# Kernel tuning notes

Measured on AMD Instinct MI355X. Metric: run time of the kernel, lower is better.

The kernel has to match this reference:

```python
import jax, jax.numpy as jnp
import numpy as np

B, INP, OUP, FGROUP, H, W = 32, 256, 256, 8, 64, 64
CG = INP // FGROUP  # channels per group in GLGF fc1 layers


def conv3x3(x, w):
    # x: (N,1,H,W), w: (1,1,3,3); stride 1, padding 1 (SAME)
    return jax.lax.conv_general_dilated(
        x, w, window_strides=(1, 1), padding='SAME',
        dimension_numbers=('NCHW', 'OIHW', 'NCHW'))


def setup_inputs() -> dict:
    key = jax.random.key(0)
    ks = jax.random.split(key, 8)
    return {
        'x': jax.random.normal(ks[0], (B, INP, H, W), dtype=jnp.float32),
        # GLGF params (all 1x1 convs, bias=False), stored as dense matrices
        'w1l': jax.random.normal(ks[1], (FGROUP, CG, CG), dtype=jnp.float32) * 0.05,   # wn_fc1_l (groups=fgroup)
        'w1g1': jax.random.normal(ks[2], (FGROUP, CG), dtype=jnp.float32) * 0.05,      # wn_fc1_g1 (inp->fgroup, groups=fgroup)
        'w1g2': jax.random.normal(ks[3], (INP, FGROUP), dtype=jnp.float32) * 0.05,     # wn_fc1_g2 (fgroup->inp dense)
        'w2l': jax.random.normal(ks[4], (INP, OUP), dtype=jnp.float32) * 0.05,         # wn_fc2_l (groups=inp): input ch i -> oup outputs
        'w2g': jax.random.normal(ks[5], (INP,), dtype=jnp.float32) * 0.05,             # wn_fc2_g (inp->1 dense)
        'conv1_w': jax.random.normal(ks[6], (1, 1, 3, 3), dtype=jnp.float32) * 0.1,
        'conv2_w': jax.random.normal(ks[7], (1, 1, 3, 3), dtype=jnp.float32) * 0.1,
    }


def reference(x, w1l, w1g1, w1g2, w2l, w2g, conv1_w, conv2_w):
    b, c, h, w_ = x.shape
    fgroup, cg, _ = w1l.shape
    oup = w2l.shape[1]

    # adaptive_avg_pool2d(x, (1,1)) -> (B, inp) descriptor
    g = x.mean(axis=(2, 3))                                   # (B, inp)
    gg = g.reshape(b, fgroup, cg)

    # GLGF: fc1_l (grouped) + fc1_g2(fc1_g1) (squeeze to fgroup then expand)
    local = jnp.einsum('bgi,goi->bgo', gg, w1l).reshape(b, c)  # (B, inp)
    glob = jnp.einsum('bgi,gi->bg', gg, w1g1) @ w1g2.T         # (B, inp)
    s = jax.nn.sigmoid(local + glob)                           # (B, inp)

    # fc2_l (groups=inp): torch channel order is (input_ch g, out j) -> g*oup + j
    # fc2_g adds a per-sample scalar to every channel
    xw = s[:, :, None] * w2l + (s @ w2g)[:, None, None]        # (B, inp, oup)
    # WA_1Conv reinterprets the flat (oup*inp) channels as (oup, inp)
    Wdyn = xw.reshape(b, oup, c)                               # (B, oup, inp)

    # grouped conv with groups=batch, ksize=1 == per-sample matmul
    y = jnp.einsum('bihw,boi->bohw', x, Wdyn)                  # (B, oup, H, W)

    # channel gating: mean over channels -> conv3x3 -> sigmoid -> conv3x3
    cmap = y.mean(axis=1, keepdims=True)                       # (B, 1, H, W)
    cmap = conv3x3(cmap, conv1_w)
    cmap = jax.nn.sigmoid(cmap)
    cmap = conv3x3(cmap, conv2_w)
    return y * cmap
```

## Files before the change

kernel.cpp:

```cpp
#include <hip/hip_runtime.h>
#include <hip/hip_bf16.h>

typedef float  f32x4  __attribute__((ext_vector_type(4)));
typedef short  bf16x8 __attribute__((ext_vector_type(8)));

__device__ __forceinline__ short f2bf(float f) {
    union { __hip_bfloat16 h; short s; } u;
    u.h = __float2bfloat16(f);
    return u.s;
}

__device__ __forceinline__ void gload_lds16(const void* g, void* l) {
    __builtin_amdgcn_global_load_lds(
        (const __attribute__((address_space(1))) unsigned int*)g,
        (__attribute__((address_space(3))) unsigned int*)l, 16, 0, 0);
}

__global__ __launch_bounds__(256) void transpose_kernel(const float* __restrict__ x,
                                                        short* __restrict__ xt,
                                                        float* __restrict__ gpart) {
    const int pchunk = blockIdx.x;
    const int c0 = blockIdx.y * 64;
    const int b  = blockIdx.z;
    const int tid = threadIdx.x;
    const int row = tid >> 2;
    const int quad = tid & 3;
    const int p0 = pchunk * 64;

    __shared__ short tile[64 * 72];

    const float* xr = x + ((size_t)(b * 256 + c0 + row)) * 4096 + p0 + quad * 16;
    float sum = 0.f;
    #pragma unroll
    for (int it = 0; it < 4; ++it) {
        float4 v = *reinterpret_cast<const float4*>(xr + it * 4);
        sum += v.x + v.y + v.z + v.w;
        int pb = quad * 16 + it * 4;
        tile[(pb + 0) * 72 + row] = f2bf(v.x);
        tile[(pb + 1) * 72 + row] = f2bf(v.y);
        tile[(pb + 2) * 72 + row] = f2bf(v.z);
        tile[(pb + 3) * 72 + row] = f2bf(v.w);
    }
    sum += __shfl_xor(sum, 1, 64);
    sum += __shfl_xor(sum, 2, 64);
    if (quad == 0) gpart[(size_t)(b * 256 + c0 + row) * 64 + pchunk] = sum;
    __syncthreads();
    int p = tid >> 2;
    const int4* src = reinterpret_cast<const int4*>(&tile[p * 72 + quad * 16]);
    int4* dst = reinterpret_cast<int4*>(xt + ((size_t)b * 4096 + p0 + p) * 256 + c0 + quad * 16);
    dst[0] = src[0];
    dst[1] = src[1];
}

__global__ __launch_bounds__(256) void prep_kernel(
    const float* __restrict__ gpart, const float* __restrict__ w1l,
    const float* __restrict__ w1g1, const float* __restrict__ w1g2,
    const float* __restrict__ w2l, const float* __restrict__ w2g,
    float* __restrict__ s_out, float* __restrict__ t_out,
    float* __restrict__ q_out, short* __restrict__ w2l_bf) {
    int b = blockIdx.x;
    int tid = threadIdx.x;
    if (b >= 32) {
        int seg = b - 32;
        const float* src = w2l + seg * 4096;
        short* dst = w2l_bf + seg * 4096;
        #pragma unroll
        for (int it = 0; it < 4; ++it) {
            float4 v = *reinterpret_cast<const float4*>(src + it * 1024 + tid * 4);
            short4 o;
            o.x = f2bf(v.x); o.y = f2bf(v.y); o.z = f2bf(v.z); o.w = f2bf(v.w);
            *reinterpret_cast<short4*>(dst + it * 1024 + tid * 4) = o;
        }
        return;
    }
    __shared__ float gs[256];
    __shared__ float zs[8];
    __shared__ float ss[256];
    __shared__ float red[4];
    {
        const float4* gp = reinterpret_cast<const float4*>(gpart + (size_t)(b * 256 + tid) * 64);
        float acc = 0.f;
        #pragma unroll
        for (int j = 0; j < 16; ++j) { float4 v = gp[j]; acc += v.x + v.y + v.z + v.w; }
        gs[tid] = acc * (1.0f / 4096.0f);
    }
    __syncthreads();
    if (tid < 8) {
        float z = 0.f;
        for (int i = 0; i < 32; ++i) z += gs[tid * 32 + i] * w1g1[tid * 32 + i];
        zs[tid] = z;
    }
    __syncthreads();
    int grp = tid >> 5, o = tid & 31;
    float local = 0.f;
    #pragma unroll 4
    for (int i = 0; i < 32; ++i) local += gs[grp * 32 + i] * w1l[grp * 1024 + o * 32 + i];
    float glob = 0.f;
    #pragma unroll
    for (int gg = 0; gg < 8; ++gg) glob += zs[gg] * w1g2[tid * 8 + gg];
    float sv = 1.0f / (1.0f + expf(-(local + glob)));
    ss[tid] = sv;
    s_out[b * 256 + tid] = sv;
    float tv = sv * w2g[tid];
    #pragma unroll
    for (int off = 32; off; off >>= 1) tv += __shfl_down(tv, off, 64);
    if ((tid & 63) == 0) red[tid >> 6] = tv;
    __syncthreads();
    float tb = red[0] + red[1] + red[2] + red[3];
    if (tid == 0) t_out[b] = tb;
    float v = 0.f;
    for (int o2 = 0; o2 < 256; ++o2) v += ss[o2] * w2l[o2 * 256 + tid];
    q_out[b * 256 + tid] = v * (1.0f / 256.0f) + tb;
}

__global__ __launch_bounds__(256) void cmap0_kernel(const float* __restrict__ x,
                                                    const float* __restrict__ q,
                                                    float* __restrict__ cmap0,
                                                    float* __restrict__ xsum) {
    int b = blockIdx.y;
    int p = blockIdx.x * 512 + threadIdx.x * 2;
    __shared__ float qs[256];
    qs[threadIdx.x] = q[b * 256 + threadIdx.x];
    __syncthreads();
    const float* xb = x + (size_t)b * 256 * 4096;
    float a0 = 0.f, a1 = 0.f, s0 = 0.f, s1 = 0.f;
    #pragma unroll 4
    for (int i = 0; i < 256; ++i) {
        float2 v = *reinterpret_cast<const float2*>(xb + (size_t)i * 4096 + p);
        float qi = qs[i];
        a0 += qi * v.x; a1 += qi * v.y;
        s0 += v.x;      s1 += v.y;
    }
    cmap0[b * 4096 + p] = a0; cmap0[b * 4096 + p + 1] = a1;
    xsum[b * 4096 + p] = s0;  xsum[b * 4096 + p + 1] = s1;
}

__global__ __launch_bounds__(256) void convs_kernel(const float* __restrict__ in,
                                                    const float* __restrict__ w9a,
                                                    const float* __restrict__ w9b,
                                                    float* __restrict__ out) {
    int b = blockIdx.x;
    int tid = threadIdx.x;
    __shared__ float img[4096];
    __shared__ float mid[4096];
    float wa[9], wb[9];
    #pragma unroll
    for (int i = 0; i < 9; ++i) { wa[i] = w9a[i]; wb[i] = w9b[i]; }
    {
        const float4* ip = reinterpret_cast<const float4*>(in + (size_t)b * 4096);
        float4* lp = reinterpret_cast<float4*>(img);
        #pragma unroll
        for (int it = 0; it < 4; ++it) lp[it * 256 + tid] = ip[it * 256 + tid];
    }
    __syncthreads();
    #pragma unroll
    for (int it = 0; it < 16; ++it) {
        int pix = it * 256 + tid;
        int y = pix >> 6, x0 = pix & 63;
        float acc = 0.f;
        #pragma unroll
        for (int dy = -1; dy <= 1; ++dy)
            #pragma unroll
            for (int dx = -1; dx <= 1; ++dx) {
                int yy = y + dy, xx = x0 + dx;
                if (yy >= 0 && yy < 64 && xx >= 0 && xx < 64)
                    acc += img[yy * 64 + xx] * wa[(dy + 1) * 3 + (dx + 1)];
            }
        mid[pix] = 1.0f / (1.0f + expf(-acc));
    }
    __syncthreads();
    #pragma unroll
    for (int it = 0; it < 16; ++it) {
        int pix = it * 256 + tid;
        int y = pix >> 6, x0 = pix & 63;
        float acc = 0.f;
        #pragma unroll
        for (int dy = -1; dy <= 1; ++dy)
            #pragma unroll
            for (int dx = -1; dx <= 1; ++dx) {
                int yy = y + dy, xx = x0 + dx;
                if (yy >= 0 && yy < 64 && xx >= 0 && xx < 64)
                    acc += mid[yy * 64 + xx] * wb[(dy + 1) * 3 + (dx + 1)];
            }
        out[(size_t)b * 4096 + pix] = acc;
    }
}

__global__ __launch_bounds__(512) void gemm_epi_kernel(
    const short* __restrict__ xt, const short* __restrict__ w2l_bf,
    const float* __restrict__ s, const float* __restrict__ t,
    const float* __restrict__ xsum, const float* __restrict__ cmap,
    float* __restrict__ out) {
    const int b  = blockIdx.z;
    const int p0 = blockIdx.x * 64;
    const int tid  = threadIdx.x;
    const int lane = tid & 63;
    const int w    = tid >> 6;
    const int wm = w >> 1, wn = w & 1;

    __shared__ short Alds[256 * 64];
    __shared__ short Xlds[64 * 64];

    const int sl   = (lane & 7) ^ (lane >> 3);
    const int lrow = lane >> 3;

    f32x4 acc[4][2] = {};

    for (int ks = 0; ks < 256; ks += 64) {
        #pragma unroll
        for (int j = 0; j < 4; ++j) {
            int chunk = w * 4 + j;
            int row = chunk * 8 + lrow;
            gload_lds16(w2l_bf + (size_t)row * 256 + ks + sl * 8,
                        (char*)Alds + chunk * 1024);
        }
        {
            int prow = w * 8 + lrow;
            gload_lds16(xt + ((size_t)b * 4096 + p0 + prow) * 256 + ks + sl * 8,
                        (char*)Xlds + w * 1024);
        }
        __syncthreads();
        #pragma unroll
        for (int kk = 0; kk < 2; ++kk) {
            bf16x8 af[4], bfr[2];
            const int ss = kk * 4 + (lane >> 4);
            #pragma unroll
            for (int m = 0; m < 4; ++m) {
                int o = wm * 64 + m * 16 + (lane & 15);
                af[m] = *reinterpret_cast<const bf16x8*>(
                    (char*)Alds + o * 128 + ((ss ^ (lane & 7)) * 16));
            }
            #pragma unroll
            for (int n = 0; n < 2; ++n) {
                int p = wn * 32 + n * 16 + (lane & 15);
                bfr[n] = *reinterpret_cast<const bf16x8*>(
                    (char*)Xlds + p * 128 + ((ss ^ (lane & 7)) * 16));
            }
            #pragma unroll
            for (int m = 0; m < 4; ++m)
                #pragma unroll
                for (int n = 0; n < 2; ++n)
                    acc[m][n] = __builtin_amdgcn_mfma_f32_16x16x32_bf16(af[m], bfr[n], acc[m][n], 0, 0, 0);
        }
        __syncthreads();
    }
    const float tb = t[b];
    #pragma unroll
    for (int n = 0; n < 2; ++n) {
        int p = p0 + wn * 32 + n * 16 + (lane & 15);
        float xs = xsum[b * 4096 + p];
        float cm = cmap[b * 4096 + p];
        float txs = tb * xs;
        #pragma unroll
        for (int m = 0; m < 4; ++m) {
            #pragma unroll
            for (int r = 0; r < 4; ++r) {
                int o = wm * 64 + m * 16 + (lane >> 4) * 4 + r;
                float yv = s[b * 256 + o] * acc[m][n][r] + txs;
                out[((size_t)b * 256 + o) * 4096 + p] = yv * cm;
            }
        }
    }
}

extern "C" void kernel_launch(void* const* d_in, const int* in_sizes, int n_in,
                              void* d_out, int out_size, void* d_ws, size_t ws_size,
                              hipStream_t stream) {
    const float* x       = (const float*)d_in[0];
    const float* w1l     = (const float*)d_in[1];
    const float* w1g1    = (const float*)d_in[2];
    const float* w1g2    = (const float*)d_in[3];
    const float* w2l     = (const float*)d_in[4];
    const float* w2g     = (const float*)d_in[5];
    const float* conv1_w = (const float*)d_in[6];
    const float* conv2_w = (const float*)d_in[7];
    float* out = (float*)d_out;

    float* wsf   = (float*)d_ws;
    float* s     = wsf;
    float* t     = wsf + 8192;
    float* q     = wsf + 8256;
    float* cmap0 = wsf + 16448;
    float* xsum  = wsf + 147520;
    float* cmap  = wsf + 278592;
    float* gpart = wsf + 409664;
    short* w2l_bf = (short*)(wsf + 933952);
    short* xt     = (short*)(wsf + 966720);

    transpose_kernel<<<dim3(64, 4, 32), 256, 0, stream>>>(x, xt, gpart);
    prep_kernel<<<48, 256, 0, stream>>>(gpart, w1l, w1g1, w1g2, w2l, w2g, s, t, q, w2l_bf);
    cmap0_kernel<<<dim3(8, 32), 256, 0, stream>>>(x, q, cmap0, xsum);
    convs_kernel<<<32, 256, 0, stream>>>(cmap0, conv1_w, conv2_w, cmap);
    gemm_epi_kernel<<<dim3(64, 1, 32), 512, 0, stream>>>(xt, w2l_bf, s, t, xsum, cmap, out);
}
```

Measured before the change: 144.0 us.

## Split cmap0 channel reduction across blocks and vectorize transpose LDS packing

The cmap0 reduction over 256 channels is split into 4 channel partitions per sample, giving 512 blocks instead of 256 and using float4 loads. Partial results are summed later in the convs and GEMM epilogue kernels. The transpose kernel now packs two channels' bf16 values into 32-bit words in a swizzled LDS tile, replacing scattered 16-bit stores. The cost is extra partial-buffer traffic and workspace, and more reads in the consumer kernels.

```diff
diff --git a/kernel.cpp b/kernel.cpp
--- a/kernel.cpp
+++ b/kernel.cpp
@@ -23,33 +23,48 @@
     const int c0 = blockIdx.y * 64;
     const int b  = blockIdx.z;
     const int tid = threadIdx.x;
-    const int row = tid >> 2;
-    const int quad = tid & 3;
+    const int cpair = tid >> 3;
+    const int poct  = tid & 7;
     const int p0 = pchunk * 64;
 
-    __shared__ short tile[64 * 72];
-
-    const float* xr = x + ((size_t)(b * 256 + c0 + row)) * 4096 + p0 + quad * 16;
-    float sum = 0.f;
-    #pragma unroll
-    for (int it = 0; it < 4; ++it) {
-        float4 v = *reinterpret_cast<const float4*>(xr + it * 4);
-        sum += v.x + v.y + v.z + v.w;
-        int pb = quad * 16 + it * 4;
-        tile[(pb + 0) * 72 + row] = f2bf(v.x);
-        tile[(pb + 1) * 72 + row] = f2bf(v.y);
-        tile[(pb + 2) * 72 + row] = f2bf(v.z);
-        tile[(pb + 3) * 72 + row] = f2bf(v.w);
-    }
-    sum += __shfl_xor(sum, 1, 64);
-    sum += __shfl_xor(sum, 2, 64);
-    if (quad == 0) gpart[(size_t)(b * 256 + c0 + row) * 64 + pchunk] = sum;
-    __syncthreads();
-    int p = tid >> 2;
-    const int4* src = reinterpret_cast<const int4*>(&tile[p * 72 + quad * 16]);
-    int4* dst = reinterpret_cast<int4*>(xt + ((size_t)b * 4096 + p0 + p) * 256 + c0 + quad * 16);
-    dst[0] = src[0];
-    dst[1] = src[1];
+    __shared__ unsigned int tile[64 * 32];
+
+    const float* rowA = x + ((size_t)(b * 256 + c0 + 2 * cpair)) * 4096 + p0 + poct * 8;
+    const float* rowB = rowA + 4096;
+    float av[8], bv[8];
+    *reinterpret_cast<float4*>(&av[0]) = *reinterpret_cast<const float4*>(rowA);
+    *reinterpret_cast<float4*>(&av[4]) = *reinterpret_cast<const float4*>(rowA + 4);
+    *reinterpret_cast<float4*>(&bv[0]) = *reinterpret_cast<const float4*>(rowB);
+    *reinterpret_cast<float4*>(&bv[4]) = *reinterpret_cast<const float4*>(rowB + 4);
+
+    float sA = 0.f, sB = 0.f;
+    #pragma unroll
+    for (int e = 0; e < 8; ++e) { sA += av[e]; sB += bv[e]; }
+    sA += __shfl_xor(sA, 1, 64); sA += __shfl_xor(sA, 2, 64); sA += __shfl_xor(sA, 4, 64);
+    sB += __shfl_xor(sB, 1, 64); sB += __shfl_xor(sB, 2, 64); sB += __shfl_xor(sB, 4, 64);
+    if (poct == 0) {
+        gpart[((size_t)(b * 256 + c0 + 2 * cpair)) * 64 + pchunk] = sA;
+        gpart[((size_t)(b * 256 + c0 + 2 * cpair + 1)) * 64 + pchunk] = sB;
+    }
+
+    const int s = cpair >> 2, w = cpair & 3;
+    #pragma unroll
+    for (int e = 0; e < 8; ++e) {
+        int p = poct * 8 + e;
+        unsigned int u = (unsigned int)(unsigned short)f2bf(av[e]) |
+                         ((unsigned int)(unsigned short)f2bf(bv[e]) << 16);
+        tile[p * 32 + ((s ^ poct) << 2) + w] = u;
+    }
+    __syncthreads();
+
+    const int so = tid & 7;
+    #pragma unroll
+    for (int h = 0; h < 2; ++h) {
+        int p = (tid >> 3) + h * 32;
+        int sp = so ^ ((p >> 3) & 7);
+        uint4 v = *reinterpret_cast<const uint4*>(&tile[p * 32 + sp * 4]);
+        *reinterpret_cast<uint4*>(xt + ((size_t)b * 4096 + p0 + p) * 256 + c0 + so * 8) = v;
+    }
 }
 
 __global__ __launch_bounds__(256) void prep_kernel(
@@ -115,27 +130,27 @@
 
 __global__ __launch_bounds__(256) void cmap0_kernel(const float* __restrict__ x,
                                                     const float* __restrict__ q,
-                                                    float* __restrict__ cmap0,
-                                                    float* __restrict__ xsum) {
-    int b = blockIdx.y;
-    int p = blockIdx.x * 512 + threadIdx.x * 2;
-    __shared__ float qs[256];
-    qs[threadIdx.x] = q[b * 256 + threadIdx.x];
-    __syncthreads();
-    const float* xb = x + (size_t)b * 256 * 4096;
-    float a0 = 0.f, a1 = 0.f, s0 = 0.f, s1 = 0.f;
-    #pragma unroll 4
-    for (int i = 0; i < 256; ++i) {
-        float2 v = *reinterpret_cast<const float2*>(xb + (size_t)i * 4096 + p);
-        float qi = qs[i];
-        a0 += qi * v.x; a1 += qi * v.y;
-        s0 += v.x;      s1 += v.y;
-    }
-    cmap0[b * 4096 + p] = a0; cmap0[b * 4096 + p + 1] = a1;
-    xsum[b * 4096 + p] = s0;  xsum[b * 4096 + p + 1] = s1;
-}
-
-__global__ __launch_bounds__(256) void convs_kernel(const float* __restrict__ in,
+                                                    float* __restrict__ cmap0p,
+                                                    float* __restrict__ xsump) {
+    const int part = blockIdx.y;
+    const int b = blockIdx.z;
+    const int p = blockIdx.x * 1024 + threadIdx.x * 4;
+    __shared__ float qs[64];
+    if (threadIdx.x < 64) qs[threadIdx.x] = q[b * 256 + part * 64 + threadIdx.x];
+    __syncthreads();
+    const float* xb = x + ((size_t)(b * 256 + part * 64)) * 4096 + p;
+    f32x4 a = {0.f, 0.f, 0.f, 0.f}, sm = {0.f, 0.f, 0.f, 0.f};
+    #pragma unroll 8
+    for (int i = 0; i < 64; ++i) {
+        f32x4 v = *reinterpret_cast<const f32x4*>(xb + (size_t)i * 4096);
+        a += qs[i] * v;
+        sm += v;
+    }
+    *reinterpret_cast<f32x4*>(cmap0p + ((size_t)(part * 32 + b)) * 4096 + p) = a;
+    *reinterpret_cast<f32x4*>(xsump  + ((size_t)(part * 32 + b)) * 4096 + p) = sm;
+}
+
+__global__ __launch_bounds__(256) void convs_kernel(const float* __restrict__ cmap0p,
                                                     const float* __restrict__ w9a,
                                                     const float* __restrict__ w9b,
                                                     float* __restrict__ out) {
@@ -147,10 +162,15 @@
     #pragma unroll
     for (int i = 0; i < 9; ++i) { wa[i] = w9a[i]; wb[i] = w9b[i]; }
     {
-        const float4* ip = reinterpret_cast<const float4*>(in + (size_t)b * 4096);
-        float4* lp = reinterpret_cast<float4*>(img);
-        #pragma unroll
-        for (int it = 0; it < 4; ++it) lp[it * 256 + tid] = ip[it * 256 + tid];
+        #pragma unroll
+        for (int it = 0; it < 4; ++it) {
+            int idx = it * 256 + tid;
+            f32x4 v = {0.f, 0.f, 0.f, 0.f};
+            #pragma unroll
+            for (int part = 0; part < 4; ++part)
+                v += *reinterpret_cast<const f32x4*>(cmap0p + ((size_t)(part * 32 + b)) * 4096 + idx * 4);
+            *reinterpret_cast<f32x4*>(&img[idx * 4]) = v;
+        }
     }
     __syncthreads();
     #pragma unroll
@@ -189,7 +209,7 @@
 __global__ __launch_bounds__(512) void gemm_epi_kernel(
     const short* __restrict__ xt, const short* __restrict__ w2l_bf,
     const float* __restrict__ s, const float* __restrict__ t,
-    const float* __restrict__ xsum, const float* __restrict__ cmap,
+    const float* __restrict__ xsump, const float* __restrict__ cmap,
     float* __restrict__ out) {
     const int b  = blockIdx.z;
     const int p0 = blockIdx.x * 64;
@@ -248,7 +268,10 @@
     #pragma unroll
     for (int n = 0; n < 2; ++n) {
         int p = p0 + wn * 32 + n * 16 + (lane & 15);
-        float xs = xsum[b * 4096 + p];
+        float xs = 0.f;
+        #pragma unroll
+        for (int part = 0; part < 4; ++part)
+            xs += xsump[((size_t)(part * 32 + b)) * 4096 + p];
         float cm = cmap[b * 4096 + p];
         float txs = tb * xs;
         #pragma unroll
@@ -276,20 +299,20 @@
     const float* conv2_w = (const float*)d_in[7];
     float* out = (float*)d_out;
 
-    float* wsf   = (float*)d_ws;
-    float* s     = wsf;
-    float* t     = wsf + 8192;
-    float* q     = wsf + 8256;
-    float* cmap0 = wsf + 16448;
-    float* xsum  = wsf + 147520;
-    float* cmap  = wsf + 278592;
-    float* gpart = wsf + 409664;
-    short* w2l_bf = (short*)(wsf + 933952);
-    short* xt     = (short*)(wsf + 966720);
+    float* wsf    = (float*)d_ws;
+    float* s      = wsf;
+    float* t      = wsf + 8192;
+    float* q      = wsf + 8256;
+    float* cmap0p = wsf + 16448;
+    float* xsump  = wsf + 540736;
+    float* cmap   = wsf + 1065024;
+    float* gpart  = wsf + 1196096;
+    short* w2l_bf = (short*)(wsf + 1720384);
+    short* xt     = (short*)(wsf + 1753152);
 
     transpose_kernel<<<dim3(64, 4, 32), 256, 0, stream>>>(x, xt, gpart);
     prep_kernel<<<48, 256, 0, stream>>>(gpart, w1l, w1g1, w1g2, w2l, w2g, s, t, q, w2l_bf);
-    cmap0_kernel<<<dim3(8, 32), 256, 0, stream>>>(x, q, cmap0, xsum);
-    convs_kernel<<<32, 256, 0, stream>>>(cmap0, conv1_w, conv2_w, cmap);
-    gemm_epi_kernel<<<dim3(64, 1, 32), 512, 0, stream>>>(xt, w2l_bf, s, t, xsum, cmap, out);
-}
+    cmap0_kernel<<<dim3(4, 4, 32), 256, 0, stream>>>(x, q, cmap0p, xsump);
+    convs_kernel<<<32, 256, 0, stream>>>(cmap0p, conv1_w, conv2_w, cmap);
+    gemm_epi_kernel<<<dim3(64, 1, 32), 512, 0, stream>>>(xt, w2l_bf, s, t, xsump, cmap, out);
+}
```

Measured after the change: 142.0 us. No clear change (-1.4%).
